# Kernel optimization log

Hardware: AMD Instinct MI355X
Metric: run time of the kernel (lower is better)

The kernel has to match this reference:

```python
import jax, jax.numpy as jnp
import numpy as np

T, B, NUM_TAGS = 256, 4096, 128


def setup_inputs() -> dict:
    key = jax.random.key(0)
    k1, k2, k3 = jax.random.split(key, 3)
    # Backpointers from the Viterbi forward pass: valid tag indices in [0, NUM_TAGS).
    backpointers = jax.random.randint(k1, (T, B, NUM_TAGS), 0, NUM_TAGS, dtype=jnp.int32)
    # Initial state: argmax tag at the last timestep, one per batch element.
    init_state = jax.random.randint(k2, (B,), 0, NUM_TAGS, dtype=jnp.int32)
    # Float values gathered at the same indices (differentiable surrogate for the tag values).
    tags_float = jax.random.normal(k3, (T, B, NUM_TAGS), dtype=jnp.float32)
    return {"tags_float": tags_float, "backpointers": backpointers, "init_state": init_state}


def reference(tags_float, backpointers, init_state):
    """Full CRF backward decode: scan the CrfDecodeBackwardRnnCell over T steps.

    Each step replicates the cell's call():
      new_tag[b] = inputs[b, state[b]]   (gather_nd)
      new state  = new_tag
    The integer backtrace chain is driven by `backpointers`; the emitted per-step
    output gathers `tags_float` at the same (b, state[b]) indices.
    """
    def step(state, xs):
        bp_t, val_t = xs                                   # [B, NUM_TAGS] each
        idx = state[:, None]                               # [B, 1]
        new_state = jnp.take_along_axis(bp_t, idx, axis=1)[:, 0]   # [B]
        val = jnp.take_along_axis(val_t, idx, axis=1)[:, 0]        # [B]
        return new_state, val

    _, vals = jax.lax.scan(step, init_state, (backpointers, tags_float))
    return vals[..., None]  # [T, B, 1], matching the cell's per-step output_size=1
```

## Files before the change

kernel.cpp:

```cpp
#include <hip/hip_runtime.h>


#define T_STEPS 256
#define BATCH   4096
#define NTAGS   128

__global__ __launch_bounds__(64) void crf_chain_kernel(
    const float* __restrict__ tags,
    const int*   __restrict__ bp,
    const int*   __restrict__ init,
    float*       __restrict__ out)
{
    const int b = blockIdx.x * blockDim.x + threadIdx.x;
    if (b >= BATCH) return;

    int s = init[b];
    const size_t row_b = (size_t)b * NTAGS;

    #pragma unroll 1
    for (int t = 0; t < T_STEPS; ++t) {
        const size_t off = (size_t)t * ((size_t)BATCH * NTAGS) + row_b + (size_t)s;
        const float v  = tags[off];
        const int   ns = bp[off];
        out[(size_t)t * BATCH + b] = v;
        s = ns;
    }
}

extern "C" void kernel_launch(void* const* d_in, const int* in_sizes, int n_in,
                              void* d_out, int out_size, void* d_ws, size_t ws_size,
                              hipStream_t stream) {
    const float* tags = (const float*)d_in[0];
    const int*   bp   = (const int*)d_in[1];
    const int*   init = (const int*)d_in[2];
    float*       out  = (float*)d_out;

    crf_chain_kernel<<<dim3(BATCH / 64), dim3(64), 0, stream>>>(tags, bp, init, out);
}
```

Measured before the change: 950.6 us.

## Assign one wavefront per batch row, prefetch backpointer rows, resolve chain via shuffles

Each 64-lane wavefront now handles one batch element. The lanes cooperatively load the whole 128-entry backpointer row for every timestep with coalesced int2 loads, prefetching one step ahead, and follow the chain through cross-lane shuffles instead of dependent scattered global loads. Visited states are recorded in shared memory. After the chain is walked, the tag values are gathered in parallel across timesteps and the output is written through a shared-memory transpose. This trades a long serial chain of dependent global loads for reading the full backpointer tensor, which multiplies the bytes read by about 64x.

```diff
diff --git a/kernel.cpp b/kernel.cpp
--- a/kernel.cpp
+++ b/kernel.cpp
@@ -4,26 +4,68 @@
 #define T_STEPS 256
 #define BATCH   4096
 #define NTAGS   128
+#define WSZ     64
+#define WARPS   4
+#define NBLOCKS (BATCH / WARPS)
 
-__global__ __launch_bounds__(64) void crf_chain_kernel(
+__global__ __launch_bounds__(256) void crf_warp_chain(
     const float* __restrict__ tags,
     const int*   __restrict__ bp,
     const int*   __restrict__ init,
     float*       __restrict__ out)
 {
-    const int b = blockIdx.x * blockDim.x + threadIdx.x;
-    if (b >= BATCH) return;
+    __shared__ unsigned char sstate[WARPS][T_STEPS];
+    __shared__ float         vbuf[WARPS][T_STEPS + 1];
+
+    const int tid  = threadIdx.x;
+    const int lane = tid & (WSZ - 1);
+    const int w    = tid >> 6;
+    const int b    = blockIdx.x * WARPS + w;
+
+    const size_t stride_t = (size_t)BATCH * NTAGS;
+    const size_t row_b    = (size_t)b * NTAGS;
+
+    const int2*  rp      = reinterpret_cast<const int2*>(bp + row_b) + lane;
+    const size_t rp_step = stride_t / 2;
 
     int s = init[b];
-    const size_t row_b = (size_t)b * NTAGS;
 
-    #pragma unroll 1
-    for (int t = 0; t < T_STEPS; ++t) {
-        const size_t off = (size_t)t * ((size_t)BATCH * NTAGS) + row_b + (size_t)s;
-        const float v  = tags[off];
-        const int   ns = bp[off];
-        out[(size_t)t * BATCH + b] = v;
-        s = ns;
+    int2 r = *rp;
+    rp += rp_step;
+
+    #pragma unroll 4
+    for (int t = 0; t < T_STEPS - 1; ++t) {
+        const int2 rn = *rp;
+        rp += rp_step;
+
+        if (lane == 0) sstate[w][t] = (unsigned char)s;
+
+        const int src = s >> 1;
+        const int lo  = __shfl(r.x, src, WSZ);
+        const int hi  = __shfl(r.y, src, WSZ);
+        s = (s & 1) ? hi : lo;
+        r = rn;
+    }
+    if (lane == 0) sstate[w][T_STEPS - 1] = (unsigned char)s;
+
+    __syncthreads();
+
+    #pragma unroll
+    for (int j = 0; j < T_STEPS / WSZ; ++j) {
+        const int t  = lane + WSZ * j;
+        const int st = (int)sstate[w][t];
+        vbuf[w][t] = tags[(size_t)t * stride_t + row_b + (size_t)st];
+    }
+
+    __syncthreads();
+
+    const int b0 = blockIdx.x * WARPS;
+    #pragma unroll
+    for (int k = 0; k < (T_STEPS * WARPS) / 256; ++k) {
+        const int idx = k * 256 + tid;
+        const int t   = idx >> 2;
+        const int bl  = idx & 3;
+        out[(size_t)t * BATCH + (size_t)(b0 + bl)] = vbuf[bl][t];
     }
 }
 
@@ -35,5 +77,5 @@
     const int*   init = (const int*)d_in[2];
     float*       out  = (float*)d_out;
 
-    crf_chain_kernel<<<dim3(BATCH / 64), dim3(64), 0, stream>>>(tags, bp, init, out);
+    crf_warp_chain<<<dim3(NBLOCKS), dim3(256), 0, stream>>>(tags, bp, init, out);
 }
```

Result: faster. 890.2 us (-6.3%).
